# Kernel optimization log

Measured on AMD Instinct MI355X. Metric: run time of the kernel, lower is better.

The kernel has to match this reference:

```python
import jax, jax.numpy as jnp
import numpy as np

N = 50000
E = 640000
F_IN = 128
HID = 128
OUT = 64


def setup_inputs() -> dict:
    key = jax.random.key(0)
    ks = jax.random.split(key, 16)
    x = jax.random.normal(ks[0], (N, F_IN), dtype=jnp.float32)
    edge_index = jax.random.randint(ks[1], (2, E), 0, N, dtype=jnp.int64)

    def lin(k, fan_in, fan_out):
        bound = 1.0 / np.sqrt(fan_in)
        kw, kb = jax.random.split(k)
        W = jax.random.uniform(kw, (fan_in, fan_out), jnp.float32, -bound, bound)
        b = jax.random.uniform(kb, (fan_out,), jnp.float32, -bound, bound)
        return W, b

    W1, b1 = lin(ks[2], F_IN, HID)
    W2, b2 = lin(ks[3], HID, HID)
    W3, b3 = lin(ks[4], HID, HID)
    Wres, bres = lin(ks[5], F_IN, HID)
    Wlin, blin = lin(ks[6], HID, OUT)
    return {"x": x, "edge_index": edge_index,
            "W1": W1, "b1": b1, "W2": W2, "b2": b2, "W3": W3, "b3": b3,
            "Wres": Wres, "bres": bres, "Wlin": Wlin, "blin": blin}


def _gcn_norm(edge_index, n):
    # GCNConv default: add self-loops, symmetric normalization D^-1/2 (A+I) D^-1/2
    src, dst = edge_index[0], edge_index[1]
    deg = jax.ops.segment_sum(jnp.ones((edge_index.shape[1],), jnp.float32), dst,
                              num_segments=n) + 1.0  # +1 for self-loop
    dinv = jax.lax.rsqrt(deg)
    norm_e = dinv[src] * dinv[dst]          # [E] edge coefficients
    norm_self = 1.0 / deg                    # [N] self-loop coefficients
    return src, dst, norm_e, norm_self


def _gcn_conv(x, W, b, src, dst, norm_e, norm_self, n):
    h = x @ W                                # [N, F_out]
    agg = jax.ops.segment_sum(h[src] * norm_e[:, None], dst, num_segments=n)
    agg = agg + h * norm_self[:, None]       # self-loop contribution
    return agg + b


def reference(x, edge_index, W1, b1, W2, b2, W3, b3, Wres, bres, Wlin, blin):
    n = x.shape[0]
    src, dst, norm_e, norm_self = _gcn_norm(edge_index, n)
    x_res = x @ Wres + bres
    h = _gcn_conv(x, W1, b1, src, dst, norm_e, norm_self, n)
    h = jax.nn.relu(h + x_res)               # dropout is identity in eval mode
    h = _gcn_conv(h, W2, b2, src, dst, norm_e, norm_self, n)
    h = jax.nn.relu(h)
    h = _gcn_conv(h, W3, b3, src, dst, norm_e, norm_self, n)
    h = jax.nn.relu(h)
    return h @ Wlin + blin
```

## Files before the change

kernel.cpp:

```cpp
#include <hip/hip_runtime.h>

typedef unsigned short ushort_t;
typedef unsigned int uint_t;

typedef __bf16 bf16x8 __attribute__((ext_vector_type(8)));
typedef float f32x4 __attribute__((ext_vector_type(4)));

union BFU { ushort_t u; __bf16 h; };

__device__ __forceinline__ float bf2f(uint_t u) {
    union { uint_t i; float f; } v; v.i = u << 16; return v.f;
}
__device__ __forceinline__ ushort_t f2bf(float f) {
    union { float f; uint_t i; } v; v.f = f;
    uint_t r = v.i + 0x7fffu + ((v.i >> 16) & 1u);
    return (ushort_t)(r >> 16);
}
__device__ __forceinline__ float loadF(const void* p, size_t i, int isBf16) {
    return isBf16 ? bf2f((uint_t)((const ushort_t*)p)[i]) : ((const float*)p)[i];
}

struct DetectArgs {
    const void* t[11];
    int elems[11];
    const int* ei;
    int* flags;
};

__device__ __forceinline__ int detect_one(const void* p, int elems) {
    const uint_t* w = (const uint_t*)p;
    int n = elems / 2; if (n > 64) n = 64;
    int cnt = 0;
    for (int k = 0; k < n; ++k) {
        uint_t f = (w[k] >> 7) & 0xFFu;
        cnt += (f >= 100u && f <= 135u);
    }
    return (cnt * 10 >= n * 6) ? 1 : 0;
}

__global__ void k_pack(DetectArgs a,
                       ushort_t* __restrict__ Tcat, ushort_t* __restrict__ T2,
                       ushort_t* __restrict__ T3, ushort_t* __restrict__ Tl,
                       int* __restrict__ deg, int N) {
    __shared__ int lflag;
    int i = blockIdx.x * blockDim.x + threadIdx.x;
    if (i < N) deg[i] = 0;
    const int SQ = 128 * 128;
    int m = (i < 4 * SQ) ? (i / SQ) : 4;
    int fid = (m == 0) ? 1 : (m == 1) ? 3 : (m == 2) ? 5 : (m == 3) ? 7 : 9;
    const void* W = a.t[fid];

    if (threadIdx.x == 0) lflag = detect_one(W, a.elems[fid]);
    if (blockIdx.x == 0 && threadIdx.x >= 64 && threadIdx.x < 75) {
        int t = threadIdx.x - 64;
        a.flags[t] = detect_one(a.t[t], a.elems[t]);
    }
    if (blockIdx.x == 0 && threadIdx.x == 75) {
        int nz = 0;
        for (int k = 0; k < 64; ++k) nz += (a.ei[2 * k + 1] != 0);
        a.flags[11] = (nz == 0) ? 1 : 0;
    }
    __syncthreads();
    int isb = lflag;

    if (i < 4 * SQ) {
        int r = i % SQ;
        int k = r / 128, f = r % 128;
        ushort_t* T = (m == 0) ? Tcat : (m == 1) ? T2 : (m == 2) ? T3 : (Tcat + SQ);
        T[f * 128 + k] = f2bf(loadF(W, (size_t)k * 128 + f, isb));
    } else if (i < 4 * SQ + 128 * 64) {
        int r = i - 4 * SQ;
        int k = r / 64, f = r % 64;
        Tl[f * 128 + k] = f2bf(loadF(W, (size_t)k * 64 + f, isb));
    }
}

__global__ void k_deg(const int* __restrict__ ei, int E, int N,
                      const int* __restrict__ flags, int* __restrict__ deg,
                      int2* __restrict__ tmp) {
    int i = blockIdx.x * blockDim.x + threadIdx.x;
    int e0 = i * 4;
    if (e0 >= E) return;
    int is64 = flags[11];
    if (e0 + 3 < E && (E & 3) == 0) {
        int d[4];
        if (is64) {
            int4 va = *(const int4*)(ei + 2 * E + 2 * e0);
            int4 vb = *(const int4*)(ei + 2 * E + 2 * e0 + 4);
            d[0] = va.x; d[1] = va.z; d[2] = vb.x; d[3] = vb.z;
        } else {
            int4 va = *(const int4*)(ei + E + e0);
            d[0] = va.x; d[1] = va.y; d[2] = va.z; d[3] = va.w;
        }
        int l[4]; bool ok[4];
#pragma unroll
        for (int k = 0; k < 4; ++k) ok[k] = (unsigned)d[k] < (unsigned)N;
#pragma unroll
        for (int k = 0; k < 4; ++k)
            l[k] = ok[k] ? atomicAdd(&deg[d[k]], 1) : 0;
        int4 t01, t23;
        t01.x = ok[0] ? d[0] : -1; t01.y = l[0];
        t01.z = ok[1] ? d[1] : -1; t01.w = l[1];
        t23.x = ok[2] ? d[2] : -1; t23.y = l[2];
        t23.z = ok[3] ? d[3] : -1; t23.w = l[3];
        *(int4*)(tmp + e0) = t01;
        *(int4*)(tmp + e0 + 2) = t23;
    } else {
        for (int e = e0; e < E && e < e0 + 4; ++e) {
            int dd = is64 ? ei[2 * E + 2 * e] : ei[E + e];
            bool ok = (unsigned)dd < (unsigned)N;
            int l = ok ? atomicAdd(&deg[dd], 1) : 0;
            tmp[e] = make_int2(ok ? dd : -1, l);
        }
    }
}


__global__ __launch_bounds__(256) void k_bsum(const int* __restrict__ deg, int n,
                                              int* __restrict__ bsum) {
    int base = blockIdx.x * 1024;
    int local = 0;
#pragma unroll
    for (int j = 0; j < 4; ++j) {
        int idx = base + threadIdx.x + j * 256;
        if (idx < n) local += deg[idx];
    }
    __shared__ int s[4];
#pragma unroll
    for (int off = 32; off; off >>= 1) local += __shfl_down(local, off, 64);
    if ((threadIdx.x & 63) == 0) s[threadIdx.x >> 6] = local;
    __syncthreads();
    if (threadIdx.x == 0) bsum[blockIdx.x] = s[0] + s[1] + s[2] + s[3];
}

__global__ __launch_bounds__(256) void k_rowptr(const int* __restrict__ deg,
                                                const int* __restrict__ bsum, int n,
                                                int* __restrict__ row_ptr,
                                                float* __restrict__ dinv,
                                                float* __restrict__ nself) {
    __shared__ int s[256];
    __shared__ int sboff;
    int t = threadIdx.x;

    if (t < 64) {
        int v = (t < blockIdx.x) ? bsum[t] : 0;
#pragma unroll
        for (int off = 32; off; off >>= 1) v += __shfl_down(v, off, 64);
        if (t == 0) sboff = v;
    }

    int base = blockIdx.x * 1024 + t * 4;
    int v0 = (base + 0 < n) ? deg[base + 0] : 0;
    int v1 = (base + 1 < n) ? deg[base + 1] : 0;
    int v2 = (base + 2 < n) ? deg[base + 2] : 0;
    int v3 = (base + 3 < n) ? deg[base + 3] : 0;
    int tot = v0 + v1 + v2 + v3;
    s[t] = tot;
    __syncthreads();
    for (int off = 1; off < 256; off <<= 1) {
        int u = (t >= off) ? s[t - off] : 0;
        __syncthreads();
        s[t] += u;
        __syncthreads();
    }
    int run = sboff + ((t == 0) ? 0 : s[t - 1]);
    int vals[4] = {v0, v1, v2, v3};
#pragma unroll
    for (int j = 0; j < 4; ++j) {
        int idx = base + j;
        if (idx < n) {
            row_ptr[idx] = run;
            run += vals[j];
            float df = (float)vals[j] + 1.0f;
            dinv[idx] = rsqrtf(df);
            nself[idx] = 1.0f / df;
        }
    }
    if (blockIdx.x == gridDim.x - 1 && t == 255) row_ptr[n] = sboff + s[255];
}

__global__ void k_scatter(const int* __restrict__ ei, int E, int N,
                          const int* __restrict__ flags,
                          const int* __restrict__ row_ptr,
                          const float* __restrict__ dinv,
                          const int2* __restrict__ tmp,
                          uint2* __restrict__ colwgt) {
    int i = blockIdx.x * blockDim.x + threadIdx.x;
    int e0 = i * 4;
    if (e0 >= E) return;
    int is64 = flags[11];
    if (e0 + 3 < E && (E & 3) == 0) {
        int s[4];
        if (is64) {
            int4 sa = *(const int4*)(ei + 2 * e0);
            int4 sb = *(const int4*)(ei + 2 * e0 + 4);
            s[0] = sa.x; s[1] = sa.z; s[2] = sb.x; s[3] = sb.z;
        } else {
            int4 sa = *(const int4*)(ei + e0);
            s[0] = sa.x; s[1] = sa.y; s[2] = sa.z; s[3] = sa.w;
        }
        int4 t01 = *(const int4*)(tmp + e0);
        int4 t23 = *(const int4*)(tmp + e0 + 2);
        int d[4] = {t01.x, t01.z, t23.x, t23.z};
        int l[4] = {t01.y, t01.w, t23.y, t23.w};
        int ss[4]; int pos[4]; float wv[4];
#pragma unroll
        for (int k = 0; k < 4; ++k)
            ss[k] = ((unsigned)s[k] < (unsigned)N) ? s[k] : 0;
#pragma unroll
        for (int k = 0; k < 4; ++k) {
            if (d[k] >= 0) {
                pos[k] = row_ptr[d[k]] + l[k];
                wv[k] = dinv[ss[k]] * dinv[d[k]];
            }
        }
#pragma unroll
        for (int k = 0; k < 4; ++k) {
            if (d[k] >= 0) {
                uint2 pk;
                pk.x = (uint_t)ss[k];
                pk.y = __float_as_uint(wv[k]);
                colwgt[pos[k]] = pk;
            }
        }
    } else {
        for (int e = e0; e < E && e < e0 + 4; ++e) {
            int sv = is64 ? ei[2 * e] : ei[e];
            int2 tv = tmp[e];
            if (tv.x >= 0) {
                int ssv = ((unsigned)sv < (unsigned)N) ? sv : 0;
                uint2 pk;
                pk.x = (uint_t)ssv;
                pk.y = __float_as_uint(dinv[ssv] * dinv[tv.x]);
                colwgt[row_ptr[tv.x] + tv.y] = pk;
            }
        }
    }
}


template <int NCT>
__device__ __forceinline__ void stage_B(const ushort_t* __restrict__ WT, uint4* lds) {
    int t = threadIdx.x;
#pragma unroll
    for (int i = 0; i < NCT; ++i) {
        int g = i * 256 + t;
        uint4 v = ((const uint4*)WT)[g];
        int col = g >> 4, k8 = g & 15;
        int c = col >> 4, l16c = col & 15;
        int kk = k8 >> 2, q = k8 & 3;
        lds[((kk * NCT + c) << 6) + (q << 4) + l16c] = v;
    }
    __syncthreads();
}

__device__ __forceinline__ void load_A1(const void* __restrict__ A, int a16,
                                        int ar, int quad, bf16x8 af[4]) {
    if (a16) {
        const ushort_t* p = (const ushort_t*)A + (size_t)ar * 128 + quad * 8;
#pragma unroll
        for (int kk = 0; kk < 4; ++kk) af[kk] = *(const bf16x8*)(p + kk * 32);
    } else {
        const float* p = (const float*)A + (size_t)ar * 128 + quad * 8;
#pragma unroll
        for (int kk = 0; kk < 4; ++kk) {
            f32x4 u0 = *(const f32x4*)(p + kk * 32);
            f32x4 u1 = *(const f32x4*)(p + kk * 32 + 4);
#pragma unroll
            for (int j = 0; j < 4; ++j) {
                BFU e;
                e.u = f2bf(u0[j]); af[kk][j] = e.h;
                e.u = f2bf(u1[j]); af[kk][j + 4] = e.h;
            }
        }
    }
}

template <int NCT>
__global__ __launch_bounds__(256, 4) void k_gemm2(const void* __restrict__ A, int aFid, int aFix,
                                                  const ushort_t* __restrict__ WT,
                                                  const void* __restrict__ bias, int bFid,
                                                  void* __restrict__ C, int cFix,
                                                  int M, const int* __restrict__ flags) {
    __shared__ uint4 lds[NCT * 256];
    stage_B<NCT>(WT, lds);

    const int F = NCT * 16;
    int t = threadIdx.x;
    int wave = t >> 6, lane = t & 63;
    int quad = lane >> 4, l16 = lane & 15;
    int row0 = blockIdx.x * 64 + wave * 16;

    int a16 = (aFid >= 0) ? flags[aFid] : aFix;
    int ar = row0 + l16; if (ar >= M) ar = M - 1;

    bf16x8 af[4];
    load_A1(A, a16, ar, quad, af);

    f32x4 acc[NCT];
#pragma unroll
    for (int c = 0; c < NCT; ++c) acc[c] = (f32x4){0.f, 0.f, 0.f, 0.f};

#pragma unroll
    for (int kk = 0; kk < 4; ++kk) {
#pragma unroll
        for (int c = 0; c < NCT; ++c) {
            bf16x8 b = *(const bf16x8*)&lds[((kk * NCT + c) << 6) + lane];
            acc[c] = __builtin_amdgcn_mfma_f32_16x16x32_bf16(af[kk], b, acc[c], 0, 0, 0);
        }
    }

    int bf = (bias && bFid >= 0) ? flags[bFid] : 1;
#pragma unroll
    for (int c = 0; c < NCT; ++c) {
        int colg = c * 16 + l16;
        float bv = bias ? loadF(bias, colg, bf) : 0.0f;
#pragma unroll
        for (int q = 0; q < 4; ++q) {
            int row = row0 + quad * 4 + q;
            if (row < M) {
                float v = acc[c][q] + bv;
                if (cFix) ((ushort_t*)C)[(size_t)row * F + colg] = f2bf(v);
                else      ((float*)C)[(size_t)row * F + colg] = v;
            }
        }
    }
}

__global__ __launch_bounds__(256, 4) void k_gemm_l1(const void* __restrict__ A,
                                                    const ushort_t* __restrict__ Tcat,
                                                    const void* __restrict__ bres,
                                                    ushort_t* __restrict__ Hout,
                                                    ushort_t* __restrict__ Xres,
                                                    int M, const int* __restrict__ flags) {
    __shared__ uint4 lds[8 * 256];
    int t = threadIdx.x;
    int wave = t >> 6, lane = t & 63;
    int quad = lane >> 4, l16 = lane & 15;
    int row0 = blockIdx.x * 64 + wave * 16;

    int a16 = flags[0];
    int ar = row0 + l16; if (ar >= M) ar = M - 1;

    bf16x8 af[4];
    load_A1(A, a16, ar, quad, af);

    stage_B<8>(Tcat, lds);
    {
        f32x4 acc[8];
#pragma unroll
        for (int c = 0; c < 8; ++c) acc[c] = (f32x4){0.f, 0.f, 0.f, 0.f};
#pragma unroll
        for (int kk = 0; kk < 4; ++kk) {
#pragma unroll
            for (int c = 0; c < 8; ++c) {
                bf16x8 b = *(const bf16x8*)&lds[((kk * 8 + c) << 6) + lane];
                acc[c] = __builtin_amdgcn_mfma_f32_16x16x32_bf16(af[kk], b, acc[c], 0, 0, 0);
            }
        }
#pragma unroll
        for (int c = 0; c < 8; ++c) {
            int colg = c * 16 + l16;
#pragma unroll
            for (int q = 0; q < 4; ++q) {
                int row = row0 + quad * 4 + q;
                if (row < M) Hout[(size_t)row * 128 + colg] = f2bf(acc[c][q]);
            }
        }
    }
    __syncthreads();

    stage_B<8>(Tcat + 128 * 128, lds);
    {
        int bf = flags[8];
        f32x4 acc[8];
#pragma unroll
        for (int c = 0; c < 8; ++c) acc[c] = (f32x4){0.f, 0.f, 0.f, 0.f};
#pragma unroll
        for (int kk = 0; kk < 4; ++kk) {
#pragma unroll
            for (int c = 0; c < 8; ++c) {
                bf16x8 b = *(const bf16x8*)&lds[((kk * 8 + c) << 6) + lane];
                acc[c] = __builtin_amdgcn_mfma_f32_16x16x32_bf16(af[kk], b, acc[c], 0, 0, 0);
            }
        }
#pragma unroll
        for (int c = 0; c < 8; ++c) {
            int colg = c * 16 + l16;
            float bv = loadF(bres, colg, bf);
#pragma unroll
            for (int q = 0; q < 4; ++q) {
                int row = row0 + quad * 4 + q;
                if (row < M) Xres[(size_t)row * 128 + colg] = f2bf(acc[c][q] + bv);
            }
        }
    }
}

__global__ __launch_bounds__(256) void k_agg(const ushort_t* __restrict__ H,
                                             const int* __restrict__ row_ptr,
                                             const uint2* __restrict__ colwgt,
                                             const float* __restrict__ nself,
                                             const void* __restrict__ bias, int bFid,
                                             const ushort_t* __restrict__ other,
                                             ushort_t* __restrict__ Out,
                                             int n, const int* __restrict__ flags) {
    int node = (blockIdx.x * blockDim.x + threadIdx.x) >> 6;
    if (node >= n) return;
    int lane = threadIdx.x & 63;
    int f = lane * 2;

    float ns = nself[node];
    size_t nidx = (size_t)node * 128 + f;

    uint_t hv = *(const uint_t*)(H + nidx);
    float a0 = bf2f(hv & 0xffffu) * ns;
    float a1 = bf2f(hv >> 16) * ns;

    int beg = row_ptr[node], end = row_ptr[node + 1];
    for (int bs = beg; bs < end; bs += 64) {
        int rem = end - bs;
        int nb = (rem < 64) ? rem : 64;
        uint2 m = (lane < nb) ? colwgt[bs + lane] : (uint2){0u, 0u};
        int c = (int)m.x;
        float w = __uint_as_float(m.y);

        for (int j = 0; j < nb; j += 16) {
            int si[16]; float wi[16]; uint_t vi[16];
#pragma unroll
            for (int q = 0; q < 16; ++q) {
                si[q] = __shfl(c, j + q, 64);
                wi[q] = __shfl(w, j + q, 64);
            }
#pragma unroll
            for (int q = 0; q < 16; ++q)
                vi[q] = *(const uint_t*)(H + (size_t)si[q] * 128 + f);
#pragma unroll
            for (int q = 0; q < 16; ++q) {
                a0 = fmaf(bf2f(vi[q] & 0xffffu), wi[q], a0);
                a1 = fmaf(bf2f(vi[q] >> 16), wi[q], a1);
            }
        }
    }

    int bfm = flags[bFid];
    a0 += loadF(bias, f, bfm);
    a1 += loadF(bias, f + 1, bfm);
    if (other) {
        uint_t ov = *(const uint_t*)(other + nidx);
        a0 += bf2f(ov & 0xffffu);
        a1 += bf2f(ov >> 16);
    }
    a0 = fmaxf(a0, 0.0f);
    a1 = fmaxf(a1, 0.0f);
    uint_t outv = (uint_t)f2bf(a0) | ((uint_t)f2bf(a1) << 16);
    *(uint_t*)(Out + nidx) = outv;
}


extern "C" void kernel_launch(void* const* d_in, const int* in_sizes, int n_in,
                              void* d_out, int out_size, void* d_ws, size_t ws_size,
                              hipStream_t stream) {
    const int N = in_sizes[0] / 128;
    const int E = in_sizes[1] / 2;

    const void* x  = d_in[0];
    const int*  ei = (const int*)d_in[1];

    char* ws = (char*)d_ws;
    size_t used = 0;
    auto alloc = [&](size_t bytes) {
        char* p = ws + used;
        used += (bytes + 255) & ~(size_t)255;
        return p;
    };

    int*   flags   = (int*)alloc(64 * 4);
    int*   deg     = (int*)alloc((size_t)N * 4);
    int*   row_ptr = (int*)alloc((size_t)(N + 1) * 4);
    float* dinv    = (float*)alloc((size_t)N * 4);
    float* nself   = (float*)alloc((size_t)N * 4);
    int2*  tmp     = (int2*)alloc((size_t)E * 8);
    uint2* colwgt  = (uint2*)alloc((size_t)E * 8);
    int*   bsum    = (int*)alloc(256 * 4);
    ushort_t* Tcat = (ushort_t*)alloc(256 * 128 * 2);
    ushort_t* T2   = (ushort_t*)alloc(128 * 128 * 2);
    ushort_t* T3   = (ushort_t*)alloc(128 * 128 * 2);
    ushort_t* Tlin = (ushort_t*)alloc(128 * 64 * 2);

    ushort_t* Hbuf = (ushort_t*)alloc((size_t)N * 128 * 2);
    ushort_t* Act1 = (ushort_t*)alloc((size_t)N * 128 * 2);
    ushort_t* Act2 = (ushort_t*)alloc((size_t)N * 128 * 2);
    ushort_t* Xres = (ushort_t*)alloc((size_t)N * 128 * 2);

    if (used > ws_size) return;

    DetectArgs da;
    for (int i = 0; i < 11; ++i) { da.t[i] = d_in[i == 0 ? 0 : i + 1]; da.elems[i] = in_sizes[i == 0 ? 0 : i + 1]; }
    da.ei = ei;
    da.flags = flags;

    const int B = 256;
    int gE4   = ((E + 3) / 4 + B - 1) / B;
    int gPack = (4 * 128 * 128 + 128 * 64) / B;
    int gGemm = (N + 63) / 64;
    int gAgg  = (N + 3) / 4;
    int nb    = (N + 1023) / 1024;

    k_pack<<<gPack, B, 0, stream>>>(da, Tcat, T2, T3, Tlin, deg, N);
    k_deg<<<gE4, B, 0, stream>>>(ei, E, N, flags, deg, tmp);
    k_bsum<<<nb, B, 0, stream>>>(deg, N, bsum);
    k_rowptr<<<nb, B, 0, stream>>>(deg, bsum, N, row_ptr, dinv, nself);
    k_scatter<<<gE4, B, 0, stream>>>(ei, E, N, flags, row_ptr, dinv, tmp, colwgt);

    k_gemm_l1<<<gGemm, B, 0, stream>>>(x, Tcat, d_in[9], Hbuf, Xres, N, flags);
    k_agg<<<gAgg, B, 0, stream>>>(Hbuf, row_ptr, colwgt, nself, d_in[3], 2,
                                  Xres, Act1, N, flags);

    k_gemm2<8><<<gGemm, B, 0, stream>>>(Act1, -1, 1, T2, nullptr, -1, Hbuf, 1, N, flags);
    k_agg<<<gAgg, B, 0, stream>>>(Hbuf, row_ptr, colwgt, nself, d_in[5], 4,
                                  nullptr, Act2, N, flags);

    k_gemm2<8><<<gGemm, B, 0, stream>>>(Act2, -1, 1, T3, nullptr, -1, Hbuf, 1, N, flags);
    k_agg<<<gAgg, B, 0, stream>>>(Hbuf, row_ptr, colwgt, nself, d_in[7], 6,
                                  nullptr, Act1, N, flags);

    k_gemm2<4><<<gGemm, B, 0, stream>>>(Act1, -1, 1, Tlin, d_in[11], 10,
                                        d_out, 0, N, flags);
}
```

Before: 300.9 us.

## Use half-wave per node with 8-byte feature loads and prefetched edge bursts

The aggregation kernel now assigns 32 lanes per node, each handling four bf16 features via 8-byte loads, so a 64-lane wave processes two nodes at once. Edge (col, weight) pairs are no longer staged through a wave-wide load and shuffles. Each lane reads them directly in bursts of 8, software-prefetching the next burst while gathering the current one. The aim is to cut shuffle overhead and idle lanes on low-degree nodes (average degree about 13), at the cost of redundant per-lane edge loads and divergence between the two nodes sharing a wave.

Measured after the change: 324.6 us. +7.9%, slower.

```diff
diff --git a/kernel.cpp b/kernel.cpp
--- a/kernel.cpp
+++ b/kernel.cpp
@@ -405,56 +405,79 @@
                                              const ushort_t* __restrict__ other,
                                              ushort_t* __restrict__ Out,
                                              int n, const int* __restrict__ flags) {
-    int node = (blockIdx.x * blockDim.x + threadIdx.x) >> 6;
+    int node = (blockIdx.x * blockDim.x + threadIdx.x) >> 5;
     if (node >= n) return;
-    int lane = threadIdx.x & 63;
-    int f = lane * 2;
+    int l32 = threadIdx.x & 31;
+    int f = l32 * 4;
 
     float ns = nself[node];
     size_t nidx = (size_t)node * 128 + f;
 
-    uint_t hv = *(const uint_t*)(H + nidx);
-    float a0 = bf2f(hv & 0xffffu) * ns;
-    float a1 = bf2f(hv >> 16) * ns;
+    uint2 hv = *(const uint2*)(H + nidx);
+    float a0 = bf2f(hv.x & 0xffffu) * ns;
+    float a1 = bf2f(hv.x >> 16) * ns;
+    float a2 = bf2f(hv.y & 0xffffu) * ns;
+    float a3 = bf2f(hv.y >> 16) * ns;
 
     int beg = row_ptr[node], end = row_ptr[node + 1];
-    for (int bs = beg; bs < end; bs += 64) {
-        int rem = end - bs;
-        int nb = (rem < 64) ? rem : 64;
-        uint2 m = (lane < nb) ? colwgt[bs + lane] : (uint2){0u, 0u};
-        int c = (int)m.x;
-        float w = __uint_as_float(m.y);
-
-        for (int j = 0; j < nb; j += 16) {
-            int si[16]; float wi[16]; uint_t vi[16];
-#pragma unroll
-            for (int q = 0; q < 16; ++q) {
-                si[q] = __shfl(c, j + q, 64);
-                wi[q] = __shfl(w, j + q, 64);
-            }
-#pragma unroll
-            for (int q = 0; q < 16; ++q)
-                vi[q] = *(const uint_t*)(H + (size_t)si[q] * 128 + f);
-#pragma unroll
-            for (int q = 0; q < 16; ++q) {
-                a0 = fmaf(bf2f(vi[q] & 0xffffu), wi[q], a0);
-                a1 = fmaf(bf2f(vi[q] >> 16), wi[q], a1);
-            }
-        }
+
+    const int BURST = 8;
+    uint2 cw[BURST];
+#pragma unroll
+    for (int q = 0; q < BURST; ++q) {
+        cw[q] = make_uint2(0u, 0u);
+        if (beg + q < end) cw[q] = colwgt[beg + q];
+    }
+
+    for (int j = beg; j < end; ) {
+        int jn = j + BURST;
+        uint2 cwn[BURST];
+#pragma unroll
+        for (int q = 0; q < BURST; ++q) {
+            cwn[q] = make_uint2(0u, 0u);
+            if (jn + q < end) cwn[q] = colwgt[jn + q];
+        }
+        uint2 v[BURST];
+#pragma unroll
+        for (int q = 0; q < BURST; ++q) { v[q].x = 0u; v[q].y = 0u; }
+#pragma unroll
+        for (int q = 0; q < BURST; ++q) {
+            if (j + q < end)
+                v[q] = *(const uint2*)(H + (size_t)cw[q].x * 128 + f);
+        }
+#pragma unroll
+        for (int q = 0; q < BURST; ++q) {
+            float w = __uint_as_float(cw[q].y);
+            a0 = fmaf(bf2f(v[q].x & 0xffffu), w, a0);
+            a1 = fmaf(bf2f(v[q].x >> 16), w, a1);
+            a2 = fmaf(bf2f(v[q].y & 0xffffu), w, a2);
+            a3 = fmaf(bf2f(v[q].y >> 16), w, a3);
+        }
+        j = jn;
+#pragma unroll
+        for (int q = 0; q < BURST; ++q) cw[q] = cwn[q];
     }
 
     int bfm = flags[bFid];
-    a0 += loadF(bias, f, bfm);
+    a0 += loadF(bias, f + 0, bfm);
     a1 += loadF(bias, f + 1, bfm);
+    a2 += loadF(bias, f + 2, bfm);
+    a3 += loadF(bias, f + 3, bfm);
     if (other) {
-        uint_t ov = *(const uint_t*)(other + nidx);
-        a0 += bf2f(ov & 0xffffu);
-        a1 += bf2f(ov >> 16);
+        uint2 ov = *(const uint2*)(other + nidx);
+        a0 += bf2f(ov.x & 0xffffu);
+        a1 += bf2f(ov.x >> 16);
+        a2 += bf2f(ov.y & 0xffffu);
+        a3 += bf2f(ov.y >> 16);
     }
     a0 = fmaxf(a0, 0.0f);
     a1 = fmaxf(a1, 0.0f);
-    uint_t outv = (uint_t)f2bf(a0) | ((uint_t)f2bf(a1) << 16);
-    *(uint_t*)(Out + nidx) = outv;
+    a2 = fmaxf(a2, 0.0f);
+    a3 = fmaxf(a3, 0.0f);
+    uint2 outv;
+    outv.x = (uint_t)f2bf(a0) | ((uint_t)f2bf(a1) << 16);
+    outv.y = (uint_t)f2bf(a2) | ((uint_t)f2bf(a3) << 16);
+    *(uint2*)(Out + nidx) = outv;
 }
 
 
@@ -504,7 +527,7 @@
     int gE4   = ((E + 3) / 4 + B - 1) / B;
     int gPack = (4 * 128 * 128 + 128 * 64) / B;
     int gGemm = (N + 63) / 64;
-    int gAgg  = (N + 3) / 4;
+    int gAgg  = (N + 7) / 8;
     int nb    = (N + 1023) / 1024;
 
     k_pack<<<gPack, B, 0, stream>>>(da, Tcat, T2, T3, Tlin, deg, N);
```

## Factor GCN normalization into GEMM row scaling and unweighted CSR aggregation

Applied to the files above, without the earlier changes.

Pre-scales each GEMM output row by dinv so aggregation becomes an unweighted neighbor sum scaled by dinv of the destination node. The CSR entry shrinks from index+weight to index only, removing per-edge weight computation in scatter and weight shuffles/FMAs in aggregation. Padding lanes read a zeroed extra row of H. It changes where bf16 rounding occurs, slightly altering numerics.

Result: faster. 284.2 us (-5.6%).

```diff
diff --git a/kernel.cpp b/kernel.cpp
--- a/kernel.cpp
+++ b/kernel.cpp
@@ -41,10 +41,11 @@
 __global__ void k_pack(DetectArgs a,
                        ushort_t* __restrict__ Tcat, ushort_t* __restrict__ T2,
                        ushort_t* __restrict__ T3, ushort_t* __restrict__ Tl,
-                       int* __restrict__ deg, int N) {
+                       int* __restrict__ deg, int N, uint_t* __restrict__ Hz) {
     __shared__ int lflag;
     int i = blockIdx.x * blockDim.x + threadIdx.x;
     if (i < N) deg[i] = 0;
+    if (blockIdx.x == 1 && threadIdx.x < 64) Hz[threadIdx.x] = 0u;
     const int SQ = 128 * 128;
     int m = (i < 4 * SQ) ? (i / SQ) : 4;
     int fid = (m == 0) ? 1 : (m == 1) ? 3 : (m == 2) ? 5 : (m == 3) ? 7 : 9;
@@ -136,8 +137,7 @@
 __global__ __launch_bounds__(256) void k_rowptr(const int* __restrict__ deg,
                                                 const int* __restrict__ bsum, int n,
                                                 int* __restrict__ row_ptr,
-                                                float* __restrict__ dinv,
-                                                float* __restrict__ nself) {
+                                                float* __restrict__ dinv) {
     __shared__ int s[256];
     __shared__ int sboff;
     int t = threadIdx.x;
@@ -173,7 +173,6 @@
             run += vals[j];
             float df = (float)vals[j] + 1.0f;
             dinv[idx] = rsqrtf(df);
-            nself[idx] = 1.0f / df;
         }
     }
     if (blockIdx.x == gridDim.x - 1 && t == 255) row_ptr[n] = sboff + s[255];
@@ -182,9 +181,8 @@
 __global__ void k_scatter(const int* __restrict__ ei, int E, int N,
                           const int* __restrict__ flags,
                           const int* __restrict__ row_ptr,
-                          const float* __restrict__ dinv,
                           const int2* __restrict__ tmp,
-                          uint2* __restrict__ colwgt) {
+                          uint_t* __restrict__ colw) {
     int i = blockIdx.x * blockDim.x + threadIdx.x;
     int e0 = i * 4;
     if (e0 >= E) return;
@@ -203,25 +201,14 @@
         int4 t23 = *(const int4*)(tmp + e0 + 2);
         int d[4] = {t01.x, t01.z, t23.x, t23.z};
         int l[4] = {t01.y, t01.w, t23.y, t23.w};
-        int ss[4]; int pos[4]; float wv[4];
+        int ss[4];
 #pragma unroll
         for (int k = 0; k < 4; ++k)
             ss[k] = ((unsigned)s[k] < (unsigned)N) ? s[k] : 0;
 #pragma unroll
         for (int k = 0; k < 4; ++k) {
-            if (d[k] >= 0) {
-                pos[k] = row_ptr[d[k]] + l[k];
-                wv[k] = dinv[ss[k]] * dinv[d[k]];
-            }
-        }
-#pragma unroll
-        for (int k = 0; k < 4; ++k) {
-            if (d[k] >= 0) {
-                uint2 pk;
-                pk.x = (uint_t)ss[k];
-                pk.y = __float_as_uint(wv[k]);
-                colwgt[pos[k]] = pk;
-            }
+            if (d[k] >= 0)
+                colw[row_ptr[d[k]] + l[k]] = (uint_t)ss[k];
         }
     } else {
         for (int e = e0; e < E && e < e0 + 4; ++e) {
@@ -229,10 +216,7 @@
             int2 tv = tmp[e];
             if (tv.x >= 0) {
                 int ssv = ((unsigned)sv < (unsigned)N) ? sv : 0;
-                uint2 pk;
-                pk.x = (uint_t)ssv;
-                pk.y = __float_as_uint(dinv[ssv] * dinv[tv.x]);
-                colwgt[row_ptr[tv.x] + tv.y] = pk;
+                colw[row_ptr[tv.x] + tv.y] = (uint_t)ssv;
             }
         }
     }
@@ -281,7 +265,8 @@
                                                   const ushort_t* __restrict__ WT,
                                                   const void* __restrict__ bias, int bFid,
                                                   void* __restrict__ C, int cFix,
-                                                  int M, const int* __restrict__ flags) {
+                                                  int M, const int* __restrict__ flags,
+                                                  const float* __restrict__ rowscale) {
     __shared__ uint4 lds[NCT * 256];
     stage_B<NCT>(WT, lds);
 
@@ -310,6 +295,13 @@
         }
     }
 
+    float rs[4];
+#pragma unroll
+    for (int q = 0; q < 4; ++q) {
+        int row = row0 + quad * 4 + q;
+        rs[q] = (rowscale && row < M) ? rowscale[row] : 1.0f;
+    }
+
     int bf = (bias && bFid >= 0) ? flags[bFid] : 1;
 #pragma unroll
     for (int c = 0; c < NCT; ++c) {
@@ -319,7 +311,7 @@
         for (int q = 0; q < 4; ++q) {
             int row = row0 + quad * 4 + q;
             if (row < M) {
-                float v = acc[c][q] + bv;
+                float v = acc[c][q] * rs[q] + bv;
                 if (cFix) ((ushort_t*)C)[(size_t)row * F + colg] = f2bf(v);
                 else      ((float*)C)[(size_t)row * F + colg] = v;
             }
@@ -332,7 +324,8 @@
                                                     const void* __restrict__ bres,
                                                     ushort_t* __restrict__ Hout,
                                                     ushort_t* __restrict__ Xres,
-                                                    int M, const int* __restrict__ flags) {
+                                                    int M, const int* __restrict__ flags,
+                                                    const float* __restrict__ dinv) {
     __shared__ uint4 lds[8 * 256];
     int t = threadIdx.x;
     int wave = t >> 6, lane = t & 63;
@@ -345,6 +338,13 @@
     bf16x8 af[4];
     load_A1(A, a16, ar, quad, af);
 
+    float rs[4];
+#pragma unroll
+    for (int q = 0; q < 4; ++q) {
+        int row = row0 + quad * 4 + q;
+        rs[q] = (row < M) ? dinv[row] : 1.0f;
+    }
+
     stage_B<8>(Tcat, lds);
     {
         f32x4 acc[8];
@@ -364,7 +364,7 @@
 #pragma unroll
             for (int q = 0; q < 4; ++q) {
                 int row = row0 + quad * 4 + q;
-                if (row < M) Hout[(size_t)row * 128 + colg] = f2bf(acc[c][q]);
+                if (row < M) Hout[(size_t)row * 128 + colg] = f2bf(acc[c][q] * rs[q]);
             }
         }
     }
@@ -399,8 +399,8 @@
 
 __global__ __launch_bounds__(256) void k_agg(const ushort_t* __restrict__ H,
                                              const int* __restrict__ row_ptr,
-                                             const uint2* __restrict__ colwgt,
-                                             const float* __restrict__ nself,
+                                             const uint_t* __restrict__ colw,
+                                             const float* __restrict__ dinv,
                                              const void* __restrict__ bias, int bFid,
                                              const ushort_t* __restrict__ other,
                                              ushort_t* __restrict__ Out,
@@ -410,51 +410,45 @@
     int lane = threadIdx.x & 63;
     int f = lane * 2;
 
-    float ns = nself[node];
     size_t nidx = (size_t)node * 128 + f;
 
     uint_t hv = *(const uint_t*)(H + nidx);
-    float a0 = bf2f(hv & 0xffffu) * ns;
-    float a1 = bf2f(hv >> 16) * ns;
+    float a0 = bf2f(hv & 0xffffu);
+    float a1 = bf2f(hv >> 16);
 
     int beg = row_ptr[node], end = row_ptr[node + 1];
     for (int bs = beg; bs < end; bs += 64) {
         int rem = end - bs;
         int nb = (rem < 64) ? rem : 64;
-        uint2 m = (lane < nb) ? colwgt[bs + lane] : (uint2){0u, 0u};
-        int c = (int)m.x;
-        float w = __uint_as_float(m.y);
+        int c = (lane < nb) ? (int)colw[bs + lane] : n;
 
         for (int j = 0; j < nb; j += 16) {
-            int si[16]; float wi[16]; uint_t vi[16];
-#pragma unroll
-            for (int q = 0; q < 16; ++q) {
-                si[q] = __shfl(c, j + q, 64);
-                wi[q] = __shfl(w, j + q, 64);
-            }
+            int si[16]; uint_t vi[16];
+#pragma unroll
+            for (int q = 0; q < 16; ++q) si[q] = __shfl(c, j + q, 64);
 #pragma unroll
             for (int q = 0; q < 16; ++q)
                 vi[q] = *(const uint_t*)(H + (size_t)si[q] * 128 + f);
 #pragma unroll
             for (int q = 0; q < 16; ++q) {
-                a0 = fmaf(bf2f(vi[q] & 0xffffu), wi[q], a0);
-                a1 = fmaf(bf2f(vi[q] >> 16), wi[q], a1);
-            }
-        }
-    }
-
+                a0 += bf2f(vi[q] & 0xffffu);
+                a1 += bf2f(vi[q] >> 16);
+            }
+        }
+    }
+
+    float dv = dinv[node];
     int bfm = flags[bFid];
-    a0 += loadF(bias, f, bfm);
-    a1 += loadF(bias, f + 1, bfm);
+    float a0o = fmaf(a0, dv, loadF(bias, f, bfm));
+    float a1o = fmaf(a1, dv, loadF(bias, f + 1, bfm));
     if (other) {
         uint_t ov = *(const uint_t*)(other + nidx);
-        a0 += bf2f(ov & 0xffffu);
-        a1 += bf2f(ov >> 16);
-    }
-    a0 = fmaxf(a0, 0.0f);
-    a1 = fmaxf(a1, 0.0f);
-    uint_t outv = (uint_t)f2bf(a0) | ((uint_t)f2bf(a1) << 16);
-    *(uint_t*)(Out + nidx) = outv;
+        a0o += bf2f(ov & 0xffffu);
+        a1o += bf2f(ov >> 16);
+    }
+    a0o = fmaxf(a0o, 0.0f);
+    a1o = fmaxf(a1o, 0.0f);
+    *(uint_t*)(Out + nidx) = (uint_t)f2bf(a0o) | ((uint_t)f2bf(a1o) << 16);
 }
 
 
@@ -479,16 +473,15 @@
     int*   deg     = (int*)alloc((size_t)N * 4);
     int*   row_ptr = (int*)alloc((size_t)(N + 1) * 4);
     float* dinv    = (float*)alloc((size_t)N * 4);
-    float* nself   = (float*)alloc((size_t)N * 4);
     int2*  tmp     = (int2*)alloc((size_t)E * 8);
-    uint2* colwgt  = (uint2*)alloc((size_t)E * 8);
+    uint_t* colw   = (uint_t*)alloc((size_t)E * 4);
     int*   bsum    = (int*)alloc(256 * 4);
     ushort_t* Tcat = (ushort_t*)alloc(256 * 128 * 2);
     ushort_t* T2   = (ushort_t*)alloc(128 * 128 * 2);
     ushort_t* T3   = (ushort_t*)alloc(128 * 128 * 2);
     ushort_t* Tlin = (ushort_t*)alloc(128 * 64 * 2);
 
-    ushort_t* Hbuf = (ushort_t*)alloc((size_t)N * 128 * 2);
+    ushort_t* Hbuf = (ushort_t*)alloc((size_t)(N + 1) * 128 * 2);
     ushort_t* Act1 = (ushort_t*)alloc((size_t)N * 128 * 2);
     ushort_t* Act2 = (ushort_t*)alloc((size_t)N * 128 * 2);
     ushort_t* Xres = (ushort_t*)alloc((size_t)N * 128 * 2);
@@ -507,24 +500,26 @@
     int gAgg  = (N + 3) / 4;
     int nb    = (N + 1023) / 1024;
 
-    k_pack<<<gPack, B, 0, stream>>>(da, Tcat, T2, T3, Tlin, deg, N);
+    uint_t* Hz = (uint_t*)(Hbuf + (size_t)N * 128);
+
+    k_pack<<<gPack, B, 0, stream>>>(da, Tcat, T2, T3, Tlin, deg, N, Hz);
     k_deg<<<gE4, B, 0, stream>>>(ei, E, N, flags, deg, tmp);
     k_bsum<<<nb, B, 0, stream>>>(deg, N, bsum);
-    k_rowptr<<<nb, B, 0, stream>>>(deg, bsum, N, row_ptr, dinv, nself);
-    k_scatter<<<gE4, B, 0, stream>>>(ei, E, N, flags, row_ptr, dinv, tmp, colwgt);
-
-    k_gemm_l1<<<gGemm, B, 0, stream>>>(x, Tcat, d_in[9], Hbuf, Xres, N, flags);
-    k_agg<<<gAgg, B, 0, stream>>>(Hbuf, row_ptr, colwgt, nself, d_in[3], 2,
+    k_rowptr<<<nb, B, 0, stream>>>(deg, bsum, N, row_ptr, dinv);
+    k_scatter<<<gE4, B, 0, stream>>>(ei, E, N, flags, row_ptr, tmp, colw);
+
+    k_gemm_l1<<<gGemm, B, 0, stream>>>(x, Tcat, d_in[9], Hbuf, Xres, N, flags, dinv);
+    k_agg<<<gAgg, B, 0, stream>>>(Hbuf, row_ptr, colw, dinv, d_in[3], 2,
                                   Xres, Act1, N, flags);
 
-    k_gemm2<8><<<gGemm, B, 0, stream>>>(Act1, -1, 1, T2, nullptr, -1, Hbuf, 1, N, flags);
-    k_agg<<<gAgg, B, 0, stream>>>(Hbuf, row_ptr, colwgt, nself, d_in[5], 4,
+    k_gemm2<8><<<gGemm, B, 0, stream>>>(Act1, -1, 1, T2, nullptr, -1, Hbuf, 1, N, flags, dinv);
+    k_agg<<<gAgg, B, 0, stream>>>(Hbuf, row_ptr, colw, dinv, d_in[5], 4,
                                   nullptr, Act2, N, flags);
 
-    k_gemm2<8><<<gGemm, B, 0, stream>>>(Act2, -1, 1, T3, nullptr, -1, Hbuf, 1, N, flags);
-    k_agg<<<gAgg, B, 0, stream>>>(Hbuf, row_ptr, colwgt, nself, d_in[7], 6,
+    k_gemm2<8><<<gGemm, B, 0, stream>>>(Act2, -1, 1, T3, nullptr, -1, Hbuf, 1, N, flags, dinv);
+    k_agg<<<gAgg, B, 0, stream>>>(Hbuf, row_ptr, colw, dinv, d_in[7], 6,
                                   nullptr, Act1, N, flags);
 
     k_gemm2<4><<<gGemm, B, 0, stream>>>(Act1, -1, 1, Tlin, d_in[11], 10,
-                                        d_out, 0, N, flags);
-}
+                                        d_out, 0, N, flags, nullptr);
+}
```
